# Kernel tuning notes

Hardware: AMD Instinct MI355X
Metric: run time of the kernel (lower is better)

Reference implementation:

```python
import jax, jax.numpy as jnp
import numpy as np

L0 = 1.0  # length scale used to normalize x before the MLP
N = 2_000_000  # collocation points


def setup_inputs() -> dict:
    key = jax.random.key(0)
    ks = jax.random.split(key, 7)
    def glorot(k, shape):
        fan_in = shape[1]
        return (jax.random.normal(k, shape, jnp.float32) / jnp.sqrt(jnp.float32(fan_in)))
    x = jax.random.uniform(ks[0], (N, 1), dtype=jnp.float32)
    W0 = glorot(ks[1], (8, 1))
    b0 = jax.random.normal(ks[2], (8,), jnp.float32) * 0.1
    W1 = glorot(ks[3], (8, 8))
    b1 = jax.random.normal(ks[4], (8,), jnp.float32) * 0.1
    W2 = glorot(ks[5], (2, 8))
    b2 = jax.random.normal(ks[6], (2,), jnp.float32) * 0.1
    return {"x": x, "W0": W0, "b0": b0, "W1": W1, "b1": b1, "W2": W2, "b2": b2}


def reference(x, W0, b0, W1, b1, W2, b2):
    # per-point forward: xs has shape (1,), returns (u, w) scalars
    def fwd(xs):
        h = xs / L0
        h = jnp.tanh(W0 @ h + b0)
        h = jnp.tanh(W1 @ h + b1)
        o = W2 @ h + b2
        return o[0], o[1]

    u_f = lambda xs: fwd(xs)[0]
    w_f = lambda xs: fwd(xs)[1]
    # nested forward-mode derivative chains, mirroring the module's jacfwd stacking
    u_x = lambda xs: jax.jacfwd(u_f)(xs)[0]
    u_xx = lambda xs: jax.jacfwd(u_x)(xs)[0]
    w_x = lambda xs: jax.jacfwd(w_f)(xs)[0]
    w_xx = lambda xs: jax.jacfwd(w_x)(xs)[0]
    w_xxx = lambda xs: jax.jacfwd(w_xx)(xs)[0]
    w_xxxx = lambda xs: jax.jacfwd(w_xxx)(xs)[0]

    def all_outs(xs):  # xs: (1,)
        return jnp.stack([
            u_f(xs), u_x(xs), u_xx(xs),
            w_f(xs), w_x(xs), w_xx(xs), w_xxx(xs), w_xxxx(xs),
        ])

    return jax.vmap(all_outs)(x)  # [N, 8] == (u,u_x,u_xx,w,w_x,w_xx,w_xxx,w_xxxx)
```

## Files before the change

### kernel.cpp

```cpp
#include <hip/hip_runtime.h>
#include <hip/hip_bf16.h>
#include <math.h>


__device__ __forceinline__ float fast_rcp(float x) {
#if __has_builtin(__builtin_amdgcn_rcpf)
    return __builtin_amdgcn_rcpf(x);
#else
    return 1.f / x;
#endif
}

__device__ __forceinline__ float fast_exp2(float x) {
#if __has_builtin(__builtin_amdgcn_exp2f)
    return __builtin_amdgcn_exp2f(x);
#else
    return exp2f(x);
#endif
}

__device__ __forceinline__ float tanh_fast(float z) {
    const float e = fast_exp2(z * 2.88539008177792681472f);
    return fmaf(-2.f, fast_rcp(e + 1.f), 1.f);
}

__global__ __launch_bounds__(256, 2) void pinn_taylor_kernel(
    const float* __restrict__ x,
    const float* __restrict__ W0, const float* __restrict__ b0,
    const float* __restrict__ W1, const float* __restrict__ b1,
    const float* __restrict__ W2, const float* __restrict__ b2,
    float* __restrict__ out, int n)
{
    const int i = blockIdx.x * blockDim.x + threadIdx.x;
    if (i >= n) return;

    const float xv = x[i];

    float g0[8], g1[8], g2[8], g3[8], g4[8];
    #pragma unroll
    for (int ii = 0; ii < 8; ++ii) {
        g0[ii] = b1[ii];
        g1[ii] = 0.f; g2[ii] = 0.f; g3[ii] = 0.f; g4[ii] = 0.f;
    }

    #pragma unroll
    for (int j = 0; j < 8; ++j) {
        const float a = W0[j];
        const float z = fmaf(a, xv, b0[j]);
        const float t = tanh_fast(z);
        const float s  = fmaf(-t, t, 1.f);
        const float T2 = -2.f * t * s;
        const float T3 = fmaf(4.f * t * t, s, -2.f * s * s);
        const float T4 = t * s * fmaf(-8.f, t * t, 16.f * s);
        const float a2 = a * a;
        const float d0 = t;
        const float d1 = a * s;
        const float d2 = a2 * T2;
        const float d3 = a2 * a * T3;
        const float d4 = a2 * a2 * T4;
        #pragma unroll
        for (int ii = 0; ii < 8; ++ii) {
            const float w = W1[ii * 8 + j];
            g0[ii] = fmaf(w, d0, g0[ii]);
            g1[ii] = fmaf(w, d1, g1[ii]);
            g2[ii] = fmaf(w, d2, g2[ii]);
            g3[ii] = fmaf(w, d3, g3[ii]);
            g4[ii] = fmaf(w, d4, g4[ii]);
        }
    }

    float ou0 = b2[0], ou1 = 0.f, ou2 = 0.f, ou3 = 0.f, ou4 = 0.f;
    float ow0 = b2[1], ow1 = 0.f, ow2 = 0.f, ow3 = 0.f, ow4 = 0.f;

    #pragma unroll
    for (int ii = 0; ii < 8; ++ii) {
        const float G1 = g1[ii], G2 = g2[ii], G3 = g3[ii], G4 = g4[ii];
        const float t = tanh_fast(g0[ii]);
        const float s  = fmaf(-t, t, 1.f);
        const float T2 = -2.f * t * s;
        const float T3 = fmaf(4.f * t * t, s, -2.f * s * s);
        const float T4 = t * s * fmaf(-8.f, t * t, 16.f * s);

        const float G1_2 = G1 * G1;
        const float d0 = t;
        const float d1 = s * G1;
        const float d2 = fmaf(T2, G1_2, s * G2);
        const float d3 = fmaf(T3, G1_2 * G1, fmaf(3.f * T2, G1 * G2, s * G3));
        const float d4 = fmaf(T4, G1_2 * G1_2,
                          fmaf(6.f * T3, G1_2 * G2,
                           fmaf(T2, fmaf(3.f, G2 * G2, 4.f * G1 * G3), s * G4)));

        const float wu = W2[ii];
        const float ww = W2[8 + ii];
        ou0 = fmaf(wu, d0, ou0); ou1 = fmaf(wu, d1, ou1); ou2 = fmaf(wu, d2, ou2);
        ou3 = fmaf(wu, d3, ou3); ou4 = fmaf(wu, d4, ou4);
        ow0 = fmaf(ww, d0, ow0); ow1 = fmaf(ww, d1, ow1); ow2 = fmaf(ww, d2, ow2);
        ow3 = fmaf(ww, d3, ow3); ow4 = fmaf(ww, d4, ow4);
    }

    float4* out4 = reinterpret_cast<float4*>(out);
    out4[2 * i + 0] = make_float4(ou0, ou1, ou2, ow0);
    out4[2 * i + 1] = make_float4(ow1, ow2, ow3, ow4);
}

extern "C" void kernel_launch(void* const* d_in, const int* in_sizes, int n_in,
                              void* d_out, int out_size, void* d_ws, size_t ws_size,
                              hipStream_t stream) {
    const float* x  = (const float*)d_in[0];
    const float* W0 = (const float*)d_in[1];
    const float* b0 = (const float*)d_in[2];
    const float* W1 = (const float*)d_in[3];
    const float* b1 = (const float*)d_in[4];
    const float* W2 = (const float*)d_in[5];
    const float* b2 = (const float*)d_in[6];
    float* out = (float*)d_out;

    const int n = in_sizes[0];
    const int block = 256;
    const int grid = (n + block - 1) / block;
    pinn_taylor_kernel<<<grid, block, 0, stream>>>(x, W0, b0, W1, b1, W2, b2, out, n);
}
```

Measured before the change: 130.4 us.

## Process two points per thread with packed float2 FMA math

Each thread now handles two collocation points, holding them in 2-wide float vectors so the compiler can emit packed FP32 FMA/mul instructions, which should roughly halve the VALU instruction count per point. It also drops accumulation of the unused u third and fourth derivatives and peels the first layer-1 iteration so it initializes instead of accumulating. In exchange it doubles register pressure per thread and halves the thread count. The transcendental ops stay scalar.

Result: faster. 109.6 us (-15.9%).

```diff
diff --git a/kernel.cpp b/kernel.cpp
--- a/kernel.cpp
+++ b/kernel.cpp
@@ -3,25 +3,26 @@
 #include <math.h>
 
 
-__device__ __forceinline__ float fast_rcp(float x) {
-#if __has_builtin(__builtin_amdgcn_rcpf)
-    return __builtin_amdgcn_rcpf(x);
-#else
-    return 1.f / x;
-#endif
+typedef float v2f __attribute__((ext_vector_type(2)));
+
+__device__ __forceinline__ v2f bc(float s) { v2f r; r.x = s; r.y = s; return r; }
+__device__ __forceinline__ v2f vfma(v2f a, v2f b, v2f c) {
+    return __builtin_elementwise_fma(a, b, c);
 }
 
-__device__ __forceinline__ float fast_exp2(float x) {
-#if __has_builtin(__builtin_amdgcn_exp2f)
-    return __builtin_amdgcn_exp2f(x);
-#else
-    return exp2f(x);
-#endif
-}
+__device__ __forceinline__ float fast_rcp(float x) { return __builtin_amdgcn_rcpf(x); }
+__device__ __forceinline__ float fast_exp2(float x) { return __builtin_amdgcn_exp2f(x); }
 
-__device__ __forceinline__ float tanh_fast(float z) {
-    const float e = fast_exp2(z * 2.88539008177792681472f);
-    return fmaf(-2.f, fast_rcp(e + 1.f), 1.f);
+__device__ __forceinline__ v2f tanh2(v2f z) {
+    const v2f a = bc(2.88539008177792681472f) * z;
+    v2f e;
+    e.x = fast_exp2(a.x);
+    e.y = fast_exp2(a.y);
+    const v2f ep1 = e + bc(1.f);
+    v2f r;
+    r.x = fast_rcp(ep1.x);
+    r.y = fast_rcp(ep1.y);
+    return vfma(bc(-2.f), r, bc(1.f));
 }
 
 __global__ __launch_bounds__(256, 2) void pinn_taylor_kernel(
@@ -31,76 +32,98 @@
     const float* __restrict__ W2, const float* __restrict__ b2,
     float* __restrict__ out, int n)
 {
-    const int i = blockIdx.x * blockDim.x + threadIdx.x;
-    if (i >= n) return;
+    const int i  = blockIdx.x * blockDim.x + threadIdx.x;
+    const int p0 = 2 * i;
+    if (p0 >= n) return;
+    const bool full = (p0 + 1 < n);
 
-    const float xv = x[i];
+    v2f xv;
+    if (full) {
+        const float2 xx = *reinterpret_cast<const float2*>(x + p0);
+        xv.x = xx.x; xv.y = xx.y;
+    } else {
+        xv.x = x[p0]; xv.y = 0.f;
+    }
 
-    float g0[8], g1[8], g2[8], g3[8], g4[8];
-    #pragma unroll
-    for (int ii = 0; ii < 8; ++ii) {
-        g0[ii] = b1[ii];
-        g1[ii] = 0.f; g2[ii] = 0.f; g3[ii] = 0.f; g4[ii] = 0.f;
-    }
+    v2f g0[8], g1[8], g2[8], g3[8], g4[8];
 
     #pragma unroll
     for (int j = 0; j < 8; ++j) {
-        const float a = W0[j];
-        const float z = fmaf(a, xv, b0[j]);
-        const float t = tanh_fast(z);
-        const float s  = fmaf(-t, t, 1.f);
-        const float T2 = -2.f * t * s;
-        const float T3 = fmaf(4.f * t * t, s, -2.f * s * s);
-        const float T4 = t * s * fmaf(-8.f, t * t, 16.f * s);
+        const float a  = W0[j];
+        const v2f   z  = vfma(bc(a), xv, bc(b0[j]));
+        const v2f   t  = tanh2(z);
+        const v2f   s  = vfma(-t, t, bc(1.f));
+        const v2f   ts = t * s;
+        const v2f   t2 = t * t;
+        const v2f   s2 = s * s;
+        const v2f   T2 = bc(-2.f) * ts;
+        const v2f   T3 = vfma(bc(4.f) * t2, s, bc(-2.f) * s2);
+        const v2f   T4 = ts * vfma(bc(-8.f), t2, bc(16.f) * s);
         const float a2 = a * a;
-        const float d0 = t;
-        const float d1 = a * s;
-        const float d2 = a2 * T2;
-        const float d3 = a2 * a * T3;
-        const float d4 = a2 * a2 * T4;
+        const float a3 = a2 * a;
+        const float a4 = a2 * a2;
+        const v2f d0 = t;
+        const v2f d1 = bc(a)  * s;
+        const v2f d2 = bc(a2) * T2;
+        const v2f d3 = bc(a3) * T3;
+        const v2f d4 = bc(a4) * T4;
         #pragma unroll
         for (int ii = 0; ii < 8; ++ii) {
             const float w = W1[ii * 8 + j];
-            g0[ii] = fmaf(w, d0, g0[ii]);
-            g1[ii] = fmaf(w, d1, g1[ii]);
-            g2[ii] = fmaf(w, d2, g2[ii]);
-            g3[ii] = fmaf(w, d3, g3[ii]);
-            g4[ii] = fmaf(w, d4, g4[ii]);
+            if (j == 0) {
+                g0[ii] = vfma(bc(w), d0, bc(b1[ii]));
+                g1[ii] = bc(w) * d1;
+                g2[ii] = bc(w) * d2;
+                g3[ii] = bc(w) * d3;
+                g4[ii] = bc(w) * d4;
+            } else {
+                g0[ii] = vfma(bc(w), d0, g0[ii]);
+                g1[ii] = vfma(bc(w), d1, g1[ii]);
+                g2[ii] = vfma(bc(w), d2, g2[ii]);
+                g3[ii] = vfma(bc(w), d3, g3[ii]);
+                g4[ii] = vfma(bc(w), d4, g4[ii]);
+            }
         }
     }
 
-    float ou0 = b2[0], ou1 = 0.f, ou2 = 0.f, ou3 = 0.f, ou4 = 0.f;
-    float ow0 = b2[1], ow1 = 0.f, ow2 = 0.f, ow3 = 0.f, ow4 = 0.f;
+    v2f ou0 = bc(b2[0]), ou1 = bc(0.f), ou2 = bc(0.f);
+    v2f ow0 = bc(b2[1]), ow1 = bc(0.f), ow2 = bc(0.f), ow3 = bc(0.f), ow4 = bc(0.f);
 
     #pragma unroll
     for (int ii = 0; ii < 8; ++ii) {
-        const float G1 = g1[ii], G2 = g2[ii], G3 = g3[ii], G4 = g4[ii];
-        const float t = tanh_fast(g0[ii]);
-        const float s  = fmaf(-t, t, 1.f);
-        const float T2 = -2.f * t * s;
-        const float T3 = fmaf(4.f * t * t, s, -2.f * s * s);
-        const float T4 = t * s * fmaf(-8.f, t * t, 16.f * s);
+        const v2f G1 = g1[ii], G2 = g2[ii], G3 = g3[ii], G4 = g4[ii];
+        const v2f t  = tanh2(g0[ii]);
+        const v2f s  = vfma(-t, t, bc(1.f));
+        const v2f ts = t * s;
+        const v2f t2 = t * t;
+        const v2f s2 = s * s;
+        const v2f T2 = bc(-2.f) * ts;
+        const v2f T3 = vfma(bc(4.f) * t2, s, bc(-2.f) * s2);
+        const v2f T4 = ts * vfma(bc(-8.f), t2, bc(16.f) * s);
 
-        const float G1_2 = G1 * G1;
-        const float d0 = t;
-        const float d1 = s * G1;
-        const float d2 = fmaf(T2, G1_2, s * G2);
-        const float d3 = fmaf(T3, G1_2 * G1, fmaf(3.f * T2, G1 * G2, s * G3));
-        const float d4 = fmaf(T4, G1_2 * G1_2,
-                          fmaf(6.f * T3, G1_2 * G2,
-                           fmaf(T2, fmaf(3.f, G2 * G2, 4.f * G1 * G3), s * G4)));
+        const v2f G1_2 = G1 * G1;
+        const v2f d0 = t;
+        const v2f d1 = s * G1;
+        const v2f d2 = vfma(T2, G1_2, s * G2);
+        const v2f d3 = vfma(T3, G1_2 * G1, vfma(bc(3.f) * T2, G1 * G2, s * G3));
+        const v2f d4 = vfma(T4, G1_2 * G1_2,
+                        vfma(bc(6.f) * T3, G1_2 * G2,
+                         vfma(T2, vfma(bc(3.f), G2 * G2, bc(4.f) * (G1 * G3)), s * G4)));
 
         const float wu = W2[ii];
         const float ww = W2[8 + ii];
-        ou0 = fmaf(wu, d0, ou0); ou1 = fmaf(wu, d1, ou1); ou2 = fmaf(wu, d2, ou2);
-        ou3 = fmaf(wu, d3, ou3); ou4 = fmaf(wu, d4, ou4);
-        ow0 = fmaf(ww, d0, ow0); ow1 = fmaf(ww, d1, ow1); ow2 = fmaf(ww, d2, ow2);
-        ow3 = fmaf(ww, d3, ow3); ow4 = fmaf(ww, d4, ow4);
+        ou0 = vfma(bc(wu), d0, ou0); ou1 = vfma(bc(wu), d1, ou1); ou2 = vfma(bc(wu), d2, ou2);
+        ow0 = vfma(bc(ww), d0, ow0); ow1 = vfma(bc(ww), d1, ow1); ow2 = vfma(bc(ww), d2, ow2);
+        ow3 = vfma(bc(ww), d3, ow3); ow4 = vfma(bc(ww), d4, ow4);
     }
 
     float4* out4 = reinterpret_cast<float4*>(out);
-    out4[2 * i + 0] = make_float4(ou0, ou1, ou2, ow0);
-    out4[2 * i + 1] = make_float4(ow1, ow2, ow3, ow4);
+    out4[4 * i + 0] = make_float4(ou0.x, ou1.x, ou2.x, ow0.x);
+    out4[4 * i + 1] = make_float4(ow1.x, ow2.x, ow3.x, ow4.x);
+    if (full) {
+        out4[4 * i + 2] = make_float4(ou0.y, ou1.y, ou2.y, ow0.y);
+        out4[4 * i + 3] = make_float4(ow1.y, ow2.y, ow3.y, ow4.y);
+    }
 }
 
 extern "C" void kernel_launch(void* const* d_in, const int* in_sizes, int n_in,
@@ -116,7 +139,8 @@
     float* out = (float*)d_out;
 
     const int n = in_sizes[0];
+    const int nthreads = (n + 1) / 2;
     const int block = 256;
-    const int grid = (n + block - 1) / block;
+    const int grid = (nthreads + block - 1) / block;
     pinn_taylor_kernel<<<grid, block, 0, stream>>>(x, W0, b0, W1, b1, W2, b2, out, n);
 }
```
